# Kernel optimization log

Measured on AMD Instinct MI355X. Metric: run time of the kernel, lower is better.

The kernel has to match this reference:

```python
import jax, jax.numpy as jnp
import numpy as np

TEMPERATURE = 1.0
PRED_PER_IM = 100
INVALID = np.arange(60, 80)  # invalid class logit indices (constant)


def setup_inputs() -> dict:
    key = jax.random.key(0)
    k1, k2, k3, k4, k5 = jax.random.split(key, 5)
    B, Q, C = 256, 1000, 81
    return {
        "pred_logits": jax.random.normal(k1, (B, Q, C), jnp.float32),
        "pred_obj": jax.random.normal(k2, (B, Q), jnp.float32),
        "pred_boxes": jax.random.uniform(k3, (B, Q, 4), jnp.float32),  # cxcywh in [0,1)
        "pred_unk": jax.random.normal(k4, (B, Q), jnp.float32),
        "target_sizes": jax.random.uniform(k5, (B, 2), jnp.float32, minval=480.0, maxval=1333.0),  # (h, w)
    }


def _postprocess(pred_logits, pred_obj, pred_boxes, pred_unk, target_sizes):
    B, Q, C = pred_logits.shape
    # mask invalid classes with a huge negative logit
    logits = pred_logits.at[:, :, INVALID].set(-1e11)
    obj_prob = jnp.exp(-TEMPERATURE * pred_obj)[..., None]            # [B,Q,1]
    prob = obj_prob * jax.nn.sigmoid(logits)                          # [B,Q,C]
    prob = prob.at[:, :, INVALID].set(0.0)
    unk = jax.nn.sigmoid(pred_unk)                                    # [B,Q]
    prob = prob * (1.0 - unk[..., None])
    prob = prob.at[:, :, -1].set(obj_prob[..., 0] * unk)              # unknown class slot
    # flattened top-k over (query, class)
    scores, idx = jax.lax.top_k(prob.reshape(B, Q * C), PRED_PER_IM)  # [B,K]
    topk_boxes = idx // C
    labels = idx % C
    # cxcywh -> xyxy
    cx, cy, w, h = jnp.split(pred_boxes, 4, axis=-1)
    xyxy = jnp.concatenate([cx - 0.5 * w, cy - 0.5 * h, cx + 0.5 * w, cy + 0.5 * h], axis=-1)
    boxes = jnp.take_along_axis(xyxy, topk_boxes[..., None], axis=1)  # [B,K,4]
    img_h, img_w = target_sizes[:, 0], target_sizes[:, 1]
    scale = jnp.stack([img_w, img_h, img_w, img_h], axis=1)           # [B,4]
    boxes = boxes * scale[:, None, :]
    return scores, labels, boxes


def reference(pred_logits, pred_obj, pred_boxes, pred_unk, target_sizes):
    return _postprocess(pred_logits, pred_obj, pred_boxes, pred_unk, target_sizes)
```

## Files before the change

kernel.cpp:

```cpp
#include <hip/hip_runtime.h>
#include <math.h>

#define BATCH  256
#define NQ     1000
#define NC     81
#define QC     81000
#define TOPK   100
#define NBINS  4096
#define CAP    6144
#define CAP2   1024
#define NT     1024
#define MARGIN 4096u

__device__ __forceinline__ float sigmoidf(float x) {
    if (x >= 0.f) return 1.f / (1.f + expf(-x));
    float e = expf(x);
    return e / (1.f + e);
}

__device__ __forceinline__ float fast_sig(float x) {
    return __builtin_amdgcn_rcpf(1.f + __expf(-x));
}

__device__ __forceinline__ unsigned ballot_append(unsigned* cnt, bool pass) {
    unsigned long long mask = __ballot(pass);
    unsigned base = 0;
    if (mask) {
        int lane   = (int)(threadIdx.x & 63);
        int leader = __ffsll((long long)mask) - 1;
        if (lane == leader) base = atomicAdd(cnt, (unsigned)__popcll(mask));
        base = __shfl(base, leader, 64);
        base += (unsigned)__popcll(mask & ((1ull << lane) - 1ull));
    }
    return base;
}

struct alignas(16) Smem {
    float    P[NQ];
    float    Pm2[NQ];
    float    op[NQ];
    float    omun[NQ];
    float    last[NQ];
    unsigned hist[NBINS];
    uint2    cand[CAP];
    uint2    cand2[CAP2];
    int      rowlist[NQ];
    unsigned nrows;
    unsigned cnt;
    unsigned cnt2;
    unsigned thr;
};

__device__ unsigned scan_threshold(Smem& s, int tid) {
    __syncthreads();
    if (tid < 64) {
        unsigned c = 0;
        #pragma unroll
        for (int j = 0; j < 64; ++j) {
            int jj = (j + tid) & 63;
            c += s.hist[tid * 64 + jj];
        }
        unsigned ssum = c;
        #pragma unroll
        for (int off = 1; off < 64; off <<= 1) {
            unsigned o = __shfl_down(ssum, off, 64);
            if (tid + off < 64) ssum += o;
        }
        unsigned long long bal = __ballot(ssum >= TOPK);
        int cb = 63 - __clzll(bal);
        unsigned tb = 0;
        if (cb >= 0) {
            unsigned S_cb = __shfl(ssum, cb, 64);
            unsigned c_cb = __shfl(c, cb, 64);
            unsigned acc  = S_cb - c_cb;
            unsigned fs = s.hist[cb * 64 + tid];
            #pragma unroll
            for (int off = 1; off < 64; off <<= 1) {
                unsigned o = __shfl_down(fs, off, 64);
                if (tid + off < 64) fs += o;
            }
            unsigned long long bal2 = __ballot(acc + fs >= TOPK);
            int fb = 63 - __clzll(bal2);
            tb = (unsigned)(cb * 64 + fb);
        }
        if (tid == 0) s.thr = tb;
    }
    __syncthreads();
    return s.thr;
}

__device__ void build_rows(Smem& s, unsigned thbits, int tid) {
    __syncthreads();
    if (tid == 0) s.nrows = 0;
    __syncthreads();
    for (int q = tid; q < NQ; q += NT) {
        bool pass = (__float_as_uint(s.Pm2[q]) >= thbits);
        unsigned p = ballot_append(&s.nrows, pass);
        if (pass) s.rowlist[p] = q;
    }
    __syncthreads();
}

__device__ void scan_fused(Smem& s, const float4* __restrict__ lg4,
                           unsigned thbits, int tid) {
    const int total = (int)s.nrows * 21;
    for (int idx = tid; idx < total; idx += NT) {
        int r  = idx / 21;
        int j  = idx - r * 21;
        int q  = s.rowlist[r];
        int e0 = NC * q;
        int i4 = ((e0 + 3) >> 2) + j;
        if (4 * i4 < e0 + NC) {
            float4 v4 = lg4[i4];
            int c = 4 * i4 - e0;
            float xs[4] = {v4.x, v4.y, v4.z, v4.w};
            #pragma unroll
            for (int k = 0; k < 4; ++k) {
                int ck = c + k, qk = q;
                if (ck >= NC) { ck -= NC; ++qk; }
                bool pass = false; unsigned u = 0;
                if (ck < 60) {
                    float Pq = s.P[qk];
                    if (__float_as_uint(Pq) >= thbits) {
                        u = __float_as_uint(Pq * fast_sig(xs[k]));
                        pass = (u >= thbits);
                    }
                }
                if (pass) atomicAdd(&s.hist[u >> 19], 1u);
                unsigned p = ballot_append(&s.cnt, pass);
                if (pass && p < CAP)
                    s.cand[p] = make_uint2(u, (unsigned)(qk * NC + ck));
            }
        }
    }
}

__device__ void collect_precise(Smem& s, const float4* __restrict__ lg4,
                                unsigned thbits, int tid) {
    const int total = (int)s.nrows * 21;
    for (int idx = tid; idx < total; idx += NT) {
        int r  = idx / 21;
        int j  = idx - r * 21;
        int q  = s.rowlist[r];
        int e0 = NC * q;
        int i4 = ((e0 + 3) >> 2) + j;
        if (4 * i4 < e0 + NC) {
            float4 v4 = lg4[i4];
            int c = 4 * i4 - e0;
            float xs[4] = {v4.x, v4.y, v4.z, v4.w};
            #pragma unroll
            for (int k = 0; k < 4; ++k) {
                int ck = c + k, qk = q;
                if (ck >= NC) { ck -= NC; ++qk; }
                if (ck < 60) {
                    unsigned u = __float_as_uint(s.P[qk] * fast_sig(xs[k]));
                    if (u >= thbits) {
                        float pv = (s.op[qk] * sigmoidf(xs[k])) * s.omun[qk];
                        unsigned p = atomicAdd(&s.cnt2, 1u);
                        if (p < CAP2)
                            s.cand2[p] = make_uint2(__float_as_uint(pv),
                                                    (unsigned)(qk * NC + ck));
                    }
                }
            }
        }
    }
}

__device__ void collect80_approx(Smem& s, unsigned thbits, int tid) {
    for (int q = tid; q < NQ; q += NT) {
        unsigned u = __float_as_uint(s.last[q]);
        bool pass = (u >= thbits);
        unsigned p = ballot_append(&s.cnt, pass);
        if (pass && p < CAP)
            s.cand[p] = make_uint2(u, (unsigned)(q * NC + 80));
    }
}

__device__ void collect80_precise(Smem& s, unsigned thbits, int tid) {
    for (int q = tid; q < NQ; q += NT) {
        unsigned u = __float_as_uint(s.last[q]);
        if (u >= thbits) {
            unsigned p = atomicAdd(&s.cnt2, 1u);
            if (p < CAP2) s.cand2[p] = make_uint2(u, (unsigned)(q * NC + 80));
        }
    }
}

__global__ __launch_bounds__(NT) void postprocess_kernel(
    const float* __restrict__ logits,
    const float* __restrict__ obj,
    const float* __restrict__ boxes,
    const float* __restrict__ unk,
    const float* __restrict__ tsz,
    float* __restrict__ out)
{
    __shared__ Smem s;
    const int b   = blockIdx.x;
    const int tid = threadIdx.x;
    const float*  lgf = logits + (size_t)b * QC;
    const float4* lg4 = (const float4*)lgf;

    *(uint4*)&s.hist[tid * 4] = make_uint4(0u, 0u, 0u, 0u);
    if (tid == 0) { s.cnt = 0; s.cnt2 = 0; }
    for (int q = tid; q < NQ; q += NT) {
        float op = expf(-obj[b * NQ + q]);
        float un = sigmoidf(unk[b * NQ + q]);
        float om = 1.f - un;
        s.op[q] = op; s.omun[q] = om; s.P[q] = op * om; s.last[q] = op * un;
    }
    __syncthreads();

    for (int q = tid; q < NQ; q += NT) {
        float pm = s.P[q];
        if (q + 1 < NQ) pm = fmaxf(pm, s.P[q + 1]);
        s.Pm2[q] = pm;
        atomicAdd(&s.hist[__float_as_uint(s.last[q]) >> 19], 1u);
    }

    unsigned t0   = scan_threshold(s, tid);
    unsigned th0m = t0 ? ((t0 << 19) - MARGIN) : 0;

    build_rows(s, th0m, tid);
    scan_fused(s, lg4, th0m, tid);
    collect80_approx(s, th0m, tid);
    __syncthreads();

    unsigned tF   = scan_threshold(s, tid);
    unsigned thCm = tF ? ((tF << 19) - MARGIN) : 0;

    unsigned total = s.cnt;
    if (total <= CAP) {
        for (int i = tid; i < (int)total; i += NT) {
            uint2 cd = s.cand[i];
            bool pass = (cd.x >= thCm);
            unsigned pvb = 0;
            if (pass) {
                unsigned q = cd.y / NC;
                unsigned c = cd.y - q * NC;
                float pv;
                if (c == 80) pv = s.last[q];
                else         pv = (s.op[q] * sigmoidf(lgf[cd.y])) * s.omun[q];
                pvb = __float_as_uint(pv);
            }
            unsigned p = ballot_append(&s.cnt2, pass);
            if (pass && p < CAP2) s.cand2[p] = make_uint2(pvb, cd.y);
        }
        __syncthreads();
    }
    if (total > CAP || s.cnt2 > CAP2) {
        __syncthreads();
        if (tid == 0) s.cnt2 = 0;
        __syncthreads();
        collect_precise(s, lg4, thCm, tid);
        collect80_precise(s, thCm, tid);
        __syncthreads();
        if (s.cnt2 > CAP2) {
            __syncthreads();
            if (tid == 0) s.cnt2 = 0;
            __syncthreads();
            collect_precise(s, lg4, tF << 19, tid);
            collect80_precise(s, tF << 19, tid);
            __syncthreads();
        }
    }

    const int m = (int)min(s.cnt2, (unsigned)CAP2);

    const float* bx = boxes + (size_t)b * NQ * 4;
    const float img_h = tsz[b * 2 + 0];
    const float img_w = tsz[b * 2 + 1];
    float* o_sc = out + (size_t)b * TOPK;
    float* o_lb = out + (size_t)BATCH * TOPK + (size_t)b * TOPK;
    float* o_bx = out + (size_t)2 * BATCH * TOPK + (size_t)b * TOPK * 4;

    for (int i = tid; i < m; i += NT) {
        uint2 ci = s.cand2[i];
        int r = 0;
        for (int j = 0; j < m; ++j) {
            uint2 cj = s.cand2[j];
            r += (cj.x > ci.x) || (cj.x == ci.x && cj.y < ci.y);
        }
        if (r < TOPK) {
            int ei = (int)ci.y;
            o_sc[r] = __uint_as_float(ci.x);
            o_lb[r] = (float)(ei % NC);
            int q = ei / NC;
            float cx = bx[q * 4 + 0];
            float cy = bx[q * 4 + 1];
            float w  = bx[q * 4 + 2];
            float h  = bx[q * 4 + 3];
            o_bx[r * 4 + 0] = (cx - 0.5f * w) * img_w;
            o_bx[r * 4 + 1] = (cy - 0.5f * h) * img_h;
            o_bx[r * 4 + 2] = (cx + 0.5f * w) * img_w;
            o_bx[r * 4 + 3] = (cy + 0.5f * h) * img_h;
        }
    }
}

extern "C" void kernel_launch(void* const* d_in, const int* in_sizes, int n_in,
                              void* d_out, int out_size, void* d_ws, size_t ws_size,
                              hipStream_t stream) {
    const float* pred_logits = (const float*)d_in[0];
    const float* pred_obj    = (const float*)d_in[1];
    const float* pred_boxes  = (const float*)d_in[2];
    const float* pred_unk    = (const float*)d_in[3];
    const float* target_sz   = (const float*)d_in[4];
    float* out = (float*)d_out;
    postprocess_kernel<<<BATCH, NT, 0, stream>>>(
        pred_logits, pred_obj, pred_boxes, pred_unk, target_sz, out);
}
```

Measured before the change: 136.8 us.

## Split per-image top-k across two half-query blocks and add merge kernel

Each image's query range is split into two halves, and each half is handled by a 512-thread block that writes a local top-100 to workspace. A second small kernel merges the two 200-candidate lists with a rank sort and writes scores, labels and scaled boxes. This doubles the block count from 256 to 512 to fill more compute units, and with less shared memory per block it may allow several blocks per unit. The cost is an extra kernel launch plus a workspace round trip. Padding the workspace with zeros when a half yields fewer than 100 candidates could produce bogus entries.

```diff
diff --git a/kernel.cpp b/kernel.cpp
--- a/kernel.cpp
+++ b/kernel.cpp
@@ -3,13 +3,16 @@
 
 #define BATCH  256
 #define NQ     1000
+#define HQ     500
 #define NC     81
 #define QC     81000
+#define HQC    40500
 #define TOPK   100
 #define NBINS  4096
-#define CAP    6144
+#define CAP    4096
 #define CAP2   1024
-#define NT     1024
+#define NT     512
+#define NT2    256
 #define MARGIN 4096u
 
 __device__ __forceinline__ float sigmoidf(float x) {
@@ -36,15 +39,15 @@
 }
 
 struct alignas(16) Smem {
-    float    P[NQ];
-    float    Pm2[NQ];
-    float    op[NQ];
-    float    omun[NQ];
-    float    last[NQ];
+    float    P[HQ];
+    float    Pm2[HQ];
+    float    op[HQ];
+    float    omun[HQ];
+    float    last[HQ];
     unsigned hist[NBINS];
     uint2    cand[CAP];
     uint2    cand2[CAP2];
-    int      rowlist[NQ];
+    int      rowlist[HQ];
     unsigned nrows;
     unsigned cnt;
     unsigned cnt2;
@@ -93,7 +96,7 @@
     __syncthreads();
     if (tid == 0) s.nrows = 0;
     __syncthreads();
-    for (int q = tid; q < NQ; q += NT) {
+    for (int q = tid; q < HQ; q += NT) {
         bool pass = (__float_as_uint(s.Pm2[q]) >= thbits);
         unsigned p = ballot_append(&s.nrows, pass);
         if (pass) s.rowlist[p] = q;
@@ -102,7 +105,7 @@
 }
 
 __device__ void scan_fused(Smem& s, const float4* __restrict__ lg4,
-                           unsigned thbits, int tid) {
+                           unsigned thbits, int tid, int q0) {
     const int total = (int)s.nrows * 21;
     for (int idx = tid; idx < total; idx += NT) {
         int r  = idx / 21;
@@ -129,14 +132,14 @@
                 if (pass) atomicAdd(&s.hist[u >> 19], 1u);
                 unsigned p = ballot_append(&s.cnt, pass);
                 if (pass && p < CAP)
-                    s.cand[p] = make_uint2(u, (unsigned)(qk * NC + ck));
+                    s.cand[p] = make_uint2(u, (unsigned)((q0 + qk) * NC + ck));
             }
         }
     }
 }
 
 __device__ void collect_precise(Smem& s, const float4* __restrict__ lg4,
-                                unsigned thbits, int tid) {
+                                unsigned thbits, int tid, int q0) {
     const int total = (int)s.nrows * 21;
     for (int idx = tid; idx < total; idx += NT) {
         int r  = idx / 21;
@@ -159,7 +162,7 @@
                         unsigned p = atomicAdd(&s.cnt2, 1u);
                         if (p < CAP2)
                             s.cand2[p] = make_uint2(__float_as_uint(pv),
-                                                    (unsigned)(qk * NC + ck));
+                                                    (unsigned)((q0 + qk) * NC + ck));
                     }
                 }
             }
@@ -167,53 +170,58 @@
     }
 }
 
-__device__ void collect80_approx(Smem& s, unsigned thbits, int tid) {
-    for (int q = tid; q < NQ; q += NT) {
+__device__ void collect80_approx(Smem& s, unsigned thbits, int tid, int q0) {
+    for (int q = tid; q < HQ; q += NT) {
         unsigned u = __float_as_uint(s.last[q]);
         bool pass = (u >= thbits);
         unsigned p = ballot_append(&s.cnt, pass);
         if (pass && p < CAP)
-            s.cand[p] = make_uint2(u, (unsigned)(q * NC + 80));
-    }
-}
-
-__device__ void collect80_precise(Smem& s, unsigned thbits, int tid) {
-    for (int q = tid; q < NQ; q += NT) {
+            s.cand[p] = make_uint2(u, (unsigned)((q0 + q) * NC + 80));
+    }
+}
+
+__device__ void collect80_precise(Smem& s, unsigned thbits, int tid, int q0) {
+    for (int q = tid; q < HQ; q += NT) {
         unsigned u = __float_as_uint(s.last[q]);
         if (u >= thbits) {
             unsigned p = atomicAdd(&s.cnt2, 1u);
-            if (p < CAP2) s.cand2[p] = make_uint2(u, (unsigned)(q * NC + 80));
-        }
-    }
-}
-
-__global__ __launch_bounds__(NT) void postprocess_kernel(
+            if (p < CAP2)
+                s.cand2[p] = make_uint2(u, (unsigned)((q0 + q) * NC + 80));
+        }
+    }
+}
+
+__global__ __launch_bounds__(NT, 4) void half_topk_kernel(
     const float* __restrict__ logits,
     const float* __restrict__ obj,
-    const float* __restrict__ boxes,
     const float* __restrict__ unk,
-    const float* __restrict__ tsz,
-    float* __restrict__ out)
+    uint2* __restrict__ ws)
 {
     __shared__ Smem s;
-    const int b   = blockIdx.x;
+    const int blk = blockIdx.x;
+    const int b   = blk >> 1;
+    const int h   = blk & 1;
+    const int q0  = h * HQ;
     const int tid = threadIdx.x;
     const float*  lgf = logits + (size_t)b * QC;
-    const float4* lg4 = (const float4*)lgf;
-
-    *(uint4*)&s.hist[tid * 4] = make_uint4(0u, 0u, 0u, 0u);
+    const float4* lg4 = (const float4*)(lgf + h * HQC);
+    uint2* wsb = ws + (size_t)blk * TOPK;
+
+    ((uint4*)s.hist)[tid]      = make_uint4(0u, 0u, 0u, 0u);
+    ((uint4*)s.hist)[tid + NT] = make_uint4(0u, 0u, 0u, 0u);
     if (tid == 0) { s.cnt = 0; s.cnt2 = 0; }
-    for (int q = tid; q < NQ; q += NT) {
-        float op = expf(-obj[b * NQ + q]);
-        float un = sigmoidf(unk[b * NQ + q]);
-        float om = 1.f - un;
-        s.op[q] = op; s.omun[q] = om; s.P[q] = op * om; s.last[q] = op * un;
-    }
-    __syncthreads();
-
-    for (int q = tid; q < NQ; q += NT) {
+    if (tid < TOPK) wsb[tid] = make_uint2(0u, 0u);
+    for (int q = tid; q < HQ; q += NT) {
+        float opv = expf(-obj[b * NQ + q0 + q]);
+        float un  = sigmoidf(unk[b * NQ + q0 + q]);
+        float om  = 1.f - un;
+        s.op[q] = opv; s.omun[q] = om; s.P[q] = opv * om; s.last[q] = opv * un;
+    }
+    __syncthreads();
+
+    for (int q = tid; q < HQ; q += NT) {
         float pm = s.P[q];
-        if (q + 1 < NQ) pm = fmaxf(pm, s.P[q + 1]);
+        if (q + 1 < HQ) pm = fmaxf(pm, s.P[q + 1]);
         s.Pm2[q] = pm;
         atomicAdd(&s.hist[__float_as_uint(s.last[q]) >> 19], 1u);
     }
@@ -222,8 +230,8 @@
     unsigned th0m = t0 ? ((t0 << 19) - MARGIN) : 0;
 
     build_rows(s, th0m, tid);
-    scan_fused(s, lg4, th0m, tid);
-    collect80_approx(s, th0m, tid);
+    scan_fused(s, lg4, th0m, tid, q0);
+    collect80_approx(s, th0m, tid, q0);
     __syncthreads();
 
     unsigned tF   = scan_threshold(s, tid);
@@ -236,11 +244,12 @@
             bool pass = (cd.x >= thCm);
             unsigned pvb = 0;
             if (pass) {
-                unsigned q = cd.y / NC;
-                unsigned c = cd.y - q * NC;
+                unsigned qg = cd.y / NC;
+                unsigned c  = cd.y - qg * NC;
+                int ql = (int)qg - q0;
                 float pv;
-                if (c == 80) pv = s.last[q];
-                else         pv = (s.op[q] * sigmoidf(lgf[cd.y])) * s.omun[q];
+                if (c == 80) pv = s.last[ql];
+                else         pv = (s.op[ql] * sigmoidf(lgf[cd.y])) * s.omun[ql];
                 pvb = __float_as_uint(pv);
             }
             unsigned p = ballot_append(&s.cnt2, pass);
@@ -252,27 +261,20 @@
         __syncthreads();
         if (tid == 0) s.cnt2 = 0;
         __syncthreads();
-        collect_precise(s, lg4, thCm, tid);
-        collect80_precise(s, thCm, tid);
+        collect_precise(s, lg4, thCm, tid, q0);
+        collect80_precise(s, thCm, tid, q0);
         __syncthreads();
         if (s.cnt2 > CAP2) {
             __syncthreads();
             if (tid == 0) s.cnt2 = 0;
             __syncthreads();
-            collect_precise(s, lg4, tF << 19, tid);
-            collect80_precise(s, tF << 19, tid);
+            collect_precise(s, lg4, tF << 19, tid, q0);
+            collect80_precise(s, tF << 19, tid, q0);
             __syncthreads();
         }
     }
 
     const int m = (int)min(s.cnt2, (unsigned)CAP2);
-
-    const float* bx = boxes + (size_t)b * NQ * 4;
-    const float img_h = tsz[b * 2 + 0];
-    const float img_w = tsz[b * 2 + 1];
-    float* o_sc = out + (size_t)b * TOPK;
-    float* o_lb = out + (size_t)BATCH * TOPK + (size_t)b * TOPK;
-    float* o_bx = out + (size_t)2 * BATCH * TOPK + (size_t)b * TOPK * 4;
 
     for (int i = tid; i < m; i += NT) {
         uint2 ci = s.cand2[i];
@@ -281,7 +283,35 @@
             uint2 cj = s.cand2[j];
             r += (cj.x > ci.x) || (cj.x == ci.x && cj.y < ci.y);
         }
+        if (r < TOPK) wsb[r] = ci;
+    }
+}
+
+__global__ __launch_bounds__(NT2) void merge_kernel(
+    const uint2* __restrict__ ws,
+    const float* __restrict__ boxes,
+    const float* __restrict__ tsz,
+    float* __restrict__ out)
+{
+    __shared__ uint2 c2[2 * TOPK];
+    const int b   = blockIdx.x;
+    const int tid = threadIdx.x;
+    if (tid < 2 * TOPK) c2[tid] = ws[(size_t)b * 2 * TOPK + tid];
+    __syncthreads();
+    if (tid < 2 * TOPK) {
+        uint2 ci = c2[tid];
+        int r = 0;
+        for (int j = 0; j < 2 * TOPK; ++j) {
+            uint2 cj = c2[j];
+            r += (cj.x > ci.x) || (cj.x == ci.x && cj.y < ci.y);
+        }
         if (r < TOPK) {
+            const float* bx = boxes + (size_t)b * NQ * 4;
+            const float img_h = tsz[b * 2 + 0];
+            const float img_w = tsz[b * 2 + 1];
+            float* o_sc = out + (size_t)b * TOPK;
+            float* o_lb = out + (size_t)BATCH * TOPK + (size_t)b * TOPK;
+            float* o_bx = out + (size_t)2 * BATCH * TOPK + (size_t)b * TOPK * 4;
             int ei = (int)ci.y;
             o_sc[r] = __uint_as_float(ci.x);
             o_lb[r] = (float)(ei % NC);
@@ -289,11 +319,11 @@
             float cx = bx[q * 4 + 0];
             float cy = bx[q * 4 + 1];
             float w  = bx[q * 4 + 2];
-            float h  = bx[q * 4 + 3];
-            o_bx[r * 4 + 0] = (cx - 0.5f * w) * img_w;
-            o_bx[r * 4 + 1] = (cy - 0.5f * h) * img_h;
-            o_bx[r * 4 + 2] = (cx + 0.5f * w) * img_w;
-            o_bx[r * 4 + 3] = (cy + 0.5f * h) * img_h;
+            float hh = bx[q * 4 + 3];
+            o_bx[r * 4 + 0] = (cx - 0.5f * w)  * img_w;
+            o_bx[r * 4 + 1] = (cy - 0.5f * hh) * img_h;
+            o_bx[r * 4 + 2] = (cx + 0.5f * w)  * img_w;
+            o_bx[r * 4 + 3] = (cy + 0.5f * hh) * img_h;
         }
     }
 }
@@ -307,6 +337,10 @@
     const float* pred_unk    = (const float*)d_in[3];
     const float* target_sz   = (const float*)d_in[4];
     float* out = (float*)d_out;
-    postprocess_kernel<<<BATCH, NT, 0, stream>>>(
-        pred_logits, pred_obj, pred_boxes, pred_unk, target_sz, out);
-}
+    uint2* ws  = (uint2*)d_ws;
+
+    half_topk_kernel<<<BATCH * 2, NT, 0, stream>>>(
+        pred_logits, pred_obj, pred_unk, ws);
+    merge_kernel<<<BATCH, NT2, 0, stream>>>(
+        ws, pred_boxes, target_sz, out);
+}
```

Measured after the change: 150.3 us. +9.8%, slower.

## Prefetch next logits chunk in scan and fold row building into per-thread registers

Applied to the files above, without the earlier changes.

The fused scan loop now software-pipelines its global loads, issuing the float4 load for the next iteration's chunk before processing the current one. Per-query prep keeps P-max and last-slot bits in registers, so the Pm2 shared array and separate build_rows/collect80 passes with their extra barriers go away. Box gathering uses a single float4 load. The cost is more live registers from the prefetch and the assumption that NQ is at most NT, since each thread now handles exactly one query.

```diff
diff --git a/kernel.cpp b/kernel.cpp
--- a/kernel.cpp
+++ b/kernel.cpp
@@ -37,7 +37,6 @@
 
 struct alignas(16) Smem {
     float    P[NQ];
-    float    Pm2[NQ];
     float    op[NQ];
     float    omun[NQ];
     float    last[NQ];
@@ -89,34 +88,40 @@
     return s.thr;
 }
 
-__device__ void build_rows(Smem& s, unsigned thbits, int tid) {
-    __syncthreads();
-    if (tid == 0) s.nrows = 0;
-    __syncthreads();
-    for (int q = tid; q < NQ; q += NT) {
-        bool pass = (__float_as_uint(s.Pm2[q]) >= thbits);
-        unsigned p = ballot_append(&s.nrows, pass);
-        if (pass) s.rowlist[p] = q;
-    }
-    __syncthreads();
+__device__ __forceinline__ void prep_chunk(Smem& s, int id, int& qo, int& e0o,
+                                           int& i4o, bool& ok) {
+    int r  = id / 21;
+    int j  = id - r * 21;
+    qo  = s.rowlist[r];
+    e0o = NC * qo;
+    int t4 = ((e0o + 3) >> 2) + j;
+    ok  = (4 * t4 < e0o + NC);
+    i4o = ok ? t4 : 0;
 }
 
 __device__ void scan_fused(Smem& s, const float4* __restrict__ lg4,
                            unsigned thbits, int tid) {
     const int total = (int)s.nrows * 21;
+    int  qc = 0, e0c = 0, i4c = 0; bool okc = false;
+    float4 vc = make_float4(0.f, 0.f, 0.f, 0.f);
+    if (tid < total) {
+        prep_chunk(s, tid, qc, e0c, i4c, okc);
+        if (okc) vc = lg4[i4c];
+    }
     for (int idx = tid; idx < total; idx += NT) {
-        int r  = idx / 21;
-        int j  = idx - r * 21;
-        int q  = s.rowlist[r];
-        int e0 = NC * q;
-        int i4 = ((e0 + 3) >> 2) + j;
-        if (4 * i4 < e0 + NC) {
-            float4 v4 = lg4[i4];
-            int c = 4 * i4 - e0;
-            float xs[4] = {v4.x, v4.y, v4.z, v4.w};
+        int  qn = 0, e0n = 0, i4n = 0; bool okn = false;
+        float4 vn = make_float4(0.f, 0.f, 0.f, 0.f);
+        int idxn = idx + NT;
+        if (idxn < total) {
+            prep_chunk(s, idxn, qn, e0n, i4n, okn);
+            if (okn) vn = lg4[i4n];
+        }
+        if (okc) {
+            int c = 4 * i4c - e0c;
+            float xs[4] = {vc.x, vc.y, vc.z, vc.w};
             #pragma unroll
             for (int k = 0; k < 4; ++k) {
-                int ck = c + k, qk = q;
+                int ck = c + k, qk = qc;
                 if (ck >= NC) { ck -= NC; ++qk; }
                 bool pass = false; unsigned u = 0;
                 if (ck < 60) {
@@ -132,6 +137,7 @@
                     s.cand[p] = make_uint2(u, (unsigned)(qk * NC + ck));
             }
         }
+        qc = qn; e0c = e0n; i4c = i4n; okc = okn; vc = vn;
     }
 }
 
@@ -139,12 +145,9 @@
                                 unsigned thbits, int tid) {
     const int total = (int)s.nrows * 21;
     for (int idx = tid; idx < total; idx += NT) {
-        int r  = idx / 21;
-        int j  = idx - r * 21;
-        int q  = s.rowlist[r];
-        int e0 = NC * q;
-        int i4 = ((e0 + 3) >> 2) + j;
-        if (4 * i4 < e0 + NC) {
+        int q, e0, i4; bool ok;
+        prep_chunk(s, idx, q, e0, i4, ok);
+        if (ok) {
             float4 v4 = lg4[i4];
             int c = 4 * i4 - e0;
             float xs[4] = {v4.x, v4.y, v4.z, v4.w};
@@ -167,16 +170,6 @@
     }
 }
 
-__device__ void collect80_approx(Smem& s, unsigned thbits, int tid) {
-    for (int q = tid; q < NQ; q += NT) {
-        unsigned u = __float_as_uint(s.last[q]);
-        bool pass = (u >= thbits);
-        unsigned p = ballot_append(&s.cnt, pass);
-        if (pass && p < CAP)
-            s.cand[p] = make_uint2(u, (unsigned)(q * NC + 80));
-    }
-}
-
 __device__ void collect80_precise(Smem& s, unsigned thbits, int tid) {
     for (int q = tid; q < NQ; q += NT) {
         unsigned u = __float_as_uint(s.last[q]);
@@ -202,29 +195,40 @@
     const float4* lg4 = (const float4*)lgf;
 
     *(uint4*)&s.hist[tid * 4] = make_uint4(0u, 0u, 0u, 0u);
-    if (tid == 0) { s.cnt = 0; s.cnt2 = 0; }
-    for (int q = tid; q < NQ; q += NT) {
-        float op = expf(-obj[b * NQ + q]);
-        float un = sigmoidf(unk[b * NQ + q]);
-        float om = 1.f - un;
-        s.op[q] = op; s.omun[q] = om; s.P[q] = op * om; s.last[q] = op * un;
+    if (tid == 0) { s.nrows = 0; s.cnt = 0; s.cnt2 = 0; }
+    float Pmine = 0.f; unsigned lastbits = 0;
+    if (tid < NQ) {
+        float opv = expf(-obj[b * NQ + tid]);
+        float un  = sigmoidf(unk[b * NQ + tid]);
+        float om  = 1.f - un;
+        float la  = opv * un;
+        Pmine     = opv * om;
+        lastbits  = __float_as_uint(la);
+        s.op[tid] = opv; s.omun[tid] = om; s.P[tid] = Pmine; s.last[tid] = la;
     }
     __syncthreads();
 
-    for (int q = tid; q < NQ; q += NT) {
-        float pm = s.P[q];
-        if (q + 1 < NQ) pm = fmaxf(pm, s.P[q + 1]);
-        s.Pm2[q] = pm;
-        atomicAdd(&s.hist[__float_as_uint(s.last[q]) >> 19], 1u);
+    float pm2 = Pmine;
+    if (tid < NQ) {
+        if (tid + 1 < NQ) pm2 = fmaxf(pm2, s.P[tid + 1]);
+        atomicAdd(&s.hist[lastbits >> 19], 1u);
     }
 
     unsigned t0   = scan_threshold(s, tid);
     unsigned th0m = t0 ? ((t0 << 19) - MARGIN) : 0;
 
-    build_rows(s, th0m, tid);
+    {
+        bool pr = (tid < NQ) && (__float_as_uint(pm2) >= th0m);
+        unsigned p = ballot_append(&s.nrows, pr);
+        if (pr) s.rowlist[p] = tid;
+        bool p80 = (tid < NQ) && (lastbits >= th0m);
+        unsigned p2 = ballot_append(&s.cnt, p80);
+        if (p80 && p2 < CAP)
+            s.cand[p2] = make_uint2(lastbits, (unsigned)(tid * NC + 80));
+    }
+    __syncthreads();
+
     scan_fused(s, lg4, th0m, tid);
-    collect80_approx(s, th0m, tid);
-    __syncthreads();
 
     unsigned tF   = scan_threshold(s, tid);
     unsigned thCm = tF ? ((tF << 19) - MARGIN) : 0;
@@ -267,7 +271,7 @@
 
     const int m = (int)min(s.cnt2, (unsigned)CAP2);
 
-    const float* bx = boxes + (size_t)b * NQ * 4;
+    const float4* bx4 = (const float4*)(boxes + (size_t)b * NQ * 4);
     const float img_h = tsz[b * 2 + 0];
     const float img_w = tsz[b * 2 + 1];
     float* o_sc = out + (size_t)b * TOPK;
@@ -286,14 +290,11 @@
             o_sc[r] = __uint_as_float(ci.x);
             o_lb[r] = (float)(ei % NC);
             int q = ei / NC;
-            float cx = bx[q * 4 + 0];
-            float cy = bx[q * 4 + 1];
-            float w  = bx[q * 4 + 2];
-            float h  = bx[q * 4 + 3];
-            o_bx[r * 4 + 0] = (cx - 0.5f * w) * img_w;
-            o_bx[r * 4 + 1] = (cy - 0.5f * h) * img_h;
-            o_bx[r * 4 + 2] = (cx + 0.5f * w) * img_w;
-            o_bx[r * 4 + 3] = (cy + 0.5f * h) * img_h;
+            float4 bb = bx4[q];
+            o_bx[r * 4 + 0] = (bb.x - 0.5f * bb.z) * img_w;
+            o_bx[r * 4 + 1] = (bb.y - 0.5f * bb.w) * img_h;
+            o_bx[r * 4 + 2] = (bb.x + 0.5f * bb.z) * img_w;
+            o_bx[r * 4 + 3] = (bb.y + 0.5f * bb.w) * img_h;
         }
     }
 }
```

Measured after the change: 136.8 us. About the same (-0.0%).
